# Performance work log

Measured on AMD Instinct MI355X. Metric: run time of the kernel, lower is better.

Reference implementation:

```python
import jax, jax.numpy as jnp
import numpy as np

SEQ, B, H, IN = 512, 64, 1024, 1024
STD = 1.0 / np.sqrt(H)

def setup_inputs() -> dict:
    key = jax.random.key(0)
    ks = jax.random.split(key, 9)
    u = lambda k, shape: jax.random.uniform(k, shape, jnp.float32, -STD, STD)
    return {
        "x": jax.random.normal(ks[0], (SEQ, B, IN), jnp.float32),
        "W_ih0": u(ks[1], (4 * H, IN)),
        "W_hh0": u(ks[2], (4 * H, H)),
        "b_ih0": u(ks[3], (4 * H,)),
        "b_hh0": u(ks[4], (4 * H,)),
        "W_ih1": u(ks[5], (4 * H, H)),
        "W_hh1": u(ks[6], (4 * H, H)),
        "b_ih1": u(ks[7], (4 * H,)),
        "b_hh1": u(ks[8], (4 * H,)),
    }

def _lstm_layer(xs, W_ih, W_hh, b_ih, b_hh):
    # xs: [T, B, in]. Precompute input projections for all steps (one big GEMM),
    # then scan the strictly-sequential recurrence.
    x_proj = jnp.einsum('tbi,gi->tbg', xs, W_ih) + b_ih + b_hh  # [T, B, 4H]
    h0 = jnp.zeros((xs.shape[1], H), xs.dtype)
    c0 = jnp.zeros((xs.shape[1], H), xs.dtype)

    def step(carry, xp):
        h, c = carry
        gates = xp + h @ W_hh.T  # [B, 4H]
        i, f, g, o = jnp.split(gates, 4, axis=1)
        c_next = jax.nn.sigmoid(f) * c + jax.nn.sigmoid(i) * jnp.tanh(g)
        h_next = jax.nn.sigmoid(o) * jnp.tanh(c_next)
        return (h_next, c_next), h_next

    (h_T, c_T), hs = jax.lax.scan(step, (h0, c0), x_proj)
    return hs, h_T, c_T  # hs: [T, B, H]

def reference(x, W_ih0, W_hh0, b_ih0, b_hh0, W_ih1, W_hh1, b_ih1, b_hh1):
    out0, h0, c0 = _lstm_layer(x, W_ih0, W_hh0, b_ih0, b_hh0)
    out1, h1, c1 = _lstm_layer(out0, W_ih1, W_hh1, b_ih1, b_hh1)
    h_n = jnp.stack([h0, h1], axis=0)  # [num_layers, B, H]
    c_n = jnp.stack([c0, c1], axis=0)
    return out1, h_n, c_n
```

## Files before the change

### kernel.cpp

```cpp
#include <hip/hip_runtime.h>

#define T_SEQ 512
#define BATCH 64
#define HDIM 1024
#define G4H 4096
#define TBROWS (T_SEQ * BATCH)
#define NBLK 128
#define UPB 8
#define CNT_STRIDE 16
#define HB (NBLK * BATCH * UPB)

using short8  = __attribute__((ext_vector_type(8))) short;
using float4v = __attribute__((ext_vector_type(4))) float;

__device__ __forceinline__ unsigned short f2bf(float f) {
    union { float f; unsigned int u; } v; v.f = f;
    return (unsigned short)((v.u + 0x7fffu + ((v.u >> 16) & 1u)) >> 16);
}
__device__ __forceinline__ float bf2f(unsigned short b) {
    union { unsigned int u; float f; } v; v.u = ((unsigned int)b) << 16;
    return v.f;
}

__global__ void k_cvt(const float* __restrict__ src, unsigned short* __restrict__ dst, int n) {
    int i = (blockIdx.x * 256 + threadIdx.x) * 4;
    if (i >= n) return;
    float4 v = *(const float4*)(src + i);
    ushort4 o;
    o.x = f2bf(v.x); o.y = f2bf(v.y); o.z = f2bf(v.z); o.w = f2bf(v.w);
    *(ushort4*)(dst + i) = o;
}

__global__ void k_bias(const float* __restrict__ a0, const float* __restrict__ b0,
                       const float* __restrict__ a1, const float* __restrict__ b1,
                       float* __restrict__ s0, float* __restrict__ s1) {
    int t = blockIdx.x * 256 + threadIdx.x;
    if (t < G4H) s0[t] = a0[t] + b0[t];
    else if (t < 2 * G4H) s1[t - G4H] = a1[t - G4H] + b1[t - G4H];
}

__global__ __launch_bounds__(256) void k_gemm_bt(
    const unsigned short* __restrict__ A,
    const unsigned short* __restrict__ B,
    const float* __restrict__ bias,
    unsigned short* __restrict__ C,
    int M, int N, int K)
{
    __shared__ __align__(16) unsigned short Asm[128 * 64];
    __shared__ __align__(16) unsigned short Bsm[128 * 64];

    const int w    = threadIdx.x >> 6;
    const int lane = threadIdx.x & 63;
    const int q    = lane >> 4, r15 = lane & 15;
    const int m0   = blockIdx.y * 128;
    const int n0   = blockIdx.x * 128;
    const int wm   = w & 1, wn = w >> 1;

    float4v acc[4][4];
#pragma unroll
    for (int i = 0; i < 4; i++)
#pragma unroll
        for (int j = 0; j < 4; j++) acc[i][j] = (float4v){0.f, 0.f, 0.f, 0.f};

    for (int k0 = 0; k0 < K; k0 += 64) {
        __syncthreads();
#pragma unroll
        for (int ii = 0; ii < 4; ii++) {
            int plin = (ii * 4 + w) * 64 + lane;
            int row  = plin >> 3;
            int gch  = (plin & 7) ^ (row & 7);
            const unsigned short* ga = A + (size_t)(m0 + row) * K + (k0 + gch * 8);
            const unsigned short* gb = B + (size_t)(n0 + row) * K + (k0 + gch * 8);
            __builtin_amdgcn_global_load_lds((const __attribute__((address_space(1))) void*)ga,
                                             (__attribute__((address_space(3))) void*)(Asm + plin * 8),
                                             16, 0, 0);
            __builtin_amdgcn_global_load_lds((const __attribute__((address_space(1))) void*)gb,
                                             (__attribute__((address_space(3))) void*)(Bsm + plin * 8),
                                             16, 0, 0);
        }
        __syncthreads();
#pragma unroll
        for (int kh = 0; kh < 2; kh++) {
            short8 af[4], bfr[4];
#pragma unroll
            for (int mi = 0; mi < 4; mi++) {
                int row = wm * 64 + mi * 16 + r15;
                int ch  = (kh * 4 + q) ^ (row & 7);
                af[mi]  = *(const short8*)(Asm + (row * 8 + ch) * 8);
            }
#pragma unroll
            for (int ni = 0; ni < 4; ni++) {
                int row = wn * 64 + ni * 16 + r15;
                int ch  = (kh * 4 + q) ^ (row & 7);
                bfr[ni] = *(const short8*)(Bsm + (row * 8 + ch) * 8);
            }
#pragma unroll
            for (int mi = 0; mi < 4; mi++)
#pragma unroll
                for (int ni = 0; ni < 4; ni++)
                    acc[mi][ni] = __builtin_amdgcn_mfma_f32_16x16x32_bf16(af[mi], bfr[ni], acc[mi][ni], 0, 0, 0);
        }
    }

#pragma unroll
    for (int ni = 0; ni < 4; ni++) {
        int col  = n0 + wn * 64 + ni * 16 + r15;
        float bv = bias[col];
#pragma unroll
        for (int mi = 0; mi < 4; mi++) {
            int rowb = m0 + wm * 64 + mi * 16 + q * 4;
#pragma unroll
            for (int rr = 0; rr < 4; rr++)
                C[(size_t)(rowb + rr) * N + col] = f2bf(acc[mi][ni][rr] + bv);
        }
    }
}

#define LD16U(dst, ptr) \
    asm volatile("global_load_dwordx4 %0, %1, off sc0 sc1" : "=v"(dst) : "v"(ptr))
#define ST16U(ptr, val) \
    asm volatile("global_store_dwordx4 %0, %1, off sc0 sc1" :: "v"(ptr), "v"(val) : "memory")

#define VMWAIT(N) do { \
    asm volatile("s_waitcnt vmcnt(" #N ")" ::: "memory"); \
    __builtin_amdgcn_sched_barrier(0); \
} while (0)

__device__ __forceinline__ void gate(const unsigned* prod, int g, unsigned tgt, int lane) {
    if (lane < 32) {
        const unsigned* f = prod + (size_t)(g * 32 + lane) * CNT_STRIDE;
        while (__hip_atomic_load(f, __ATOMIC_RELAXED, __HIP_MEMORY_SCOPE_AGENT) < tgt)
            __builtin_amdgcn_s_sleep(1);
    }
    __builtin_amdgcn_sched_barrier(0);
}

__device__ __forceinline__ void issue_grp(const unsigned short* hb, const unsigned short* lb,
                                          short8 (&H)[8], short8 (&L)[8]) {
#pragma unroll
    for (int i = 0; i < 8; i++) {
        LD16U(H[i], hb + i * 2048);
        LD16U(L[i], lb + i * 2048);
    }
}

__device__ __forceinline__ void mfma_grp(int g, const short8 (&ah)[8], const short8 (&al)[8],
                                         const unsigned short* Whi, const unsigned short* Wlo,
                                         int q, int r15, float4v (&acc)[2][3])
{
#pragma unroll
    for (int i = 0; i < 8; i++) {
        const int kc = g * 8 + i;
#pragma unroll
        for (int jg = 0; jg < 2; jg++) {
            const unsigned short* bb = Whi + jg * 16 * HDIM + (kc * 4 + q) * 128 + r15 * 8;
            const unsigned short* bl = Wlo + jg * 16 * HDIM + (kc * 4 + q) * 128 + r15 * 8;
            short8 bh  = *(const short8*)bb;
            short8 blv = *(const short8*)bl;
            acc[jg][0] = __builtin_amdgcn_mfma_f32_16x16x32_bf16(ah[i], bh,  acc[jg][0], 0, 0, 0);
            acc[jg][1] = __builtin_amdgcn_mfma_f32_16x16x32_bf16(al[i], bh,  acc[jg][1], 0, 0, 0);
            acc[jg][2] = __builtin_amdgcn_mfma_f32_16x16x32_bf16(ah[i], blv, acc[jg][2], 0, 0, 0);
        }
    }
}

__global__ __launch_bounds__(256) void k_lstm(
    const float* __restrict__ Whh,
    const unsigned short* __restrict__ xproj,
    unsigned short* __restrict__ h_hi,
    unsigned short* __restrict__ h_lo,
    unsigned short* __restrict__ out_b,
    float* __restrict__ out_f,
    float* __restrict__ hn, float* __restrict__ cn,
    unsigned* __restrict__ bar,
    int bar_base)
{
    extern __shared__ char smem[];
    unsigned short* Whi = (unsigned short*)smem;
    unsigned short* Wlo = Whi + 32 * HDIM;
    float* glds         = (float*)(Wlo + 32 * HDIM);
    unsigned short* stg_hi = (unsigned short*)(glds + 64 * 33);
    unsigned short* stg_lo = stg_hi + 64 * 8;

    const int nb   = blockIdx.x;
    const int tid  = threadIdx.x;
    const int w    = tid >> 6;
    const int lane = tid & 63;
    const int q    = lane >> 4, r15 = lane & 15;
    const int brow = w * 16 + r15;

    unsigned* prod = bar;
    unsigned* done = bar + NBLK * CNT_STRIDE;

    {
        int j    = tid >> 3;
        int g    = j >> 3, ui = j & 7;
        int jg   = j >> 4, jloc = j & 15;
        size_t grow = (size_t)(g * HDIM + nb * UPB + ui) * HDIM;
        unsigned short* whiB = Whi + jg * 16 * HDIM;
        unsigned short* wloB = Wlo + jg * 16 * HDIM;
        int kbase = (tid & 7) * 128;
        for (int e = 0; e < 128; e += 4) {
            int k = kbase + e;
            float4 wv = *(const float4*)(Whh + grow + k);
            float vv[4] = {wv.x, wv.y, wv.z, wv.w};
            unsigned short hs[4], ls[4];
#pragma unroll
            for (int m = 0; m < 4; m++) {
                hs[m] = f2bf(vv[m]);
                ls[m] = f2bf(vv[m] - bf2f(hs[m]));
            }
            int addr = (k >> 3) * 128 + jloc * 8 + (k & 7);
            *(ushort4*)(whiB + addr) = (ushort4){hs[0], hs[1], hs[2], hs[3]};
            *(ushort4*)(wloB + addr) = (ushort4){ls[0], ls[1], ls[2], ls[3]};
        }
    }

    const int b_act = tid >> 2;
    const int u0    = (tid & 3) * 2;
    float c0 = 0.f, c1 = 0.f;

    ushort2 xpv[4];
    {
        const unsigned short* xpb = xproj + (size_t)b_act * G4H + nb * UPB + u0;
#pragma unroll
        for (int g = 0; g < 4; g++) xpv[g] = *(const ushort2*)(xpb + g * HDIM);
    }

    __syncthreads();

    for (int t = 0; t < T_SEQ; t++) {
        const int cur = t & 1, nxt = cur ^ 1;
        const unsigned tgt = (unsigned)(bar_base + t);

        unsigned done_pre = NBLK;
        if (t >= 2 && tid < 64)
            done_pre = __hip_atomic_load(done + (size_t)(bar_base + t - 1) * CNT_STRIDE,
                                         __ATOMIC_RELAXED, __HIP_MEMORY_SCOPE_AGENT);

        float4v acc[2][3];
#pragma unroll
        for (int jg = 0; jg < 2; jg++)
#pragma unroll
            for (int p = 0; p < 3; p++) acc[jg][p] = (float4v){0.f, 0.f, 0.f, 0.f};

        if (t > 0) {
            const unsigned short* hbase = h_hi + (size_t)cur * HB + q * 512 + brow * 8;
            const unsigned short* lbase = h_lo + (size_t)cur * HB + q * 512 + brow * 8;
            short8 H0[8], L0[8], H1[8], L1[8];
            const int g0 = nb & 3;
            const int gA = g0, gB = (g0 + 1) & 3, gC = (g0 + 2) & 3, gD = (g0 + 3) & 3;

            gate(prod, gA, tgt, lane);
            issue_grp(hbase + gA * 16384, lbase + gA * 16384, H0, L0);
            gate(prod, gB, tgt, lane);
            issue_grp(hbase + gB * 16384, lbase + gB * 16384, H1, L1);
            VMWAIT(16);
            mfma_grp(gA, H0, L0, Whi, Wlo, q, r15, acc);
            gate(prod, gC, tgt, lane);
            issue_grp(hbase + gC * 16384, lbase + gC * 16384, H0, L0);
            VMWAIT(16);
            mfma_grp(gB, H1, L1, Whi, Wlo, q, r15, acc);
            gate(prod, gD, tgt, lane);
            issue_grp(hbase + gD * 16384, lbase + gD * 16384, H1, L1);
            VMWAIT(16);
            mfma_grp(gC, H0, L0, Whi, Wlo, q, r15, acc);
            VMWAIT(0);
            mfma_grp(gD, H1, L1, Whi, Wlo, q, r15, acc);
        }

#pragma unroll
        for (int jg = 0; jg < 2; jg++) {
            int browg = w * 16 + q * 4;
#pragma unroll
            for (int rr = 0; rr < 4; rr++)
                glds[(browg + rr) * 33 + jg * 16 + r15] = acc[jg][0][rr] + acc[jg][1][rr] + acc[jg][2][rr];
        }
        __syncthreads();

        if (t > 0 && tid == 0)
            __hip_atomic_fetch_add(done + (size_t)(bar_base + t) * CNT_STRIDE, 1u,
                                   __ATOMIC_RELAXED, __HIP_MEMORY_SCOPE_AGENT);

        float hv0, hv1;
        {
            const float* gr = glds + b_act * 33;
            float gi0 = gr[0*8 + u0]     + bf2f(xpv[0].x);
            float gi1 = gr[0*8 + u0 + 1] + bf2f(xpv[0].y);
            float gf0 = gr[1*8 + u0]     + bf2f(xpv[1].x);
            float gf1 = gr[1*8 + u0 + 1] + bf2f(xpv[1].y);
            float gg0 = gr[2*8 + u0]     + bf2f(xpv[2].x);
            float gg1 = gr[2*8 + u0 + 1] + bf2f(xpv[2].y);
            float go0 = gr[3*8 + u0]     + bf2f(xpv[3].x);
            float go1 = gr[3*8 + u0 + 1] + bf2f(xpv[3].y);

            c0 = (1.f / (1.f + __expf(-gf0))) * c0 + (1.f / (1.f + __expf(-gi0))) * tanhf(gg0);
            c1 = (1.f / (1.f + __expf(-gf1))) * c1 + (1.f / (1.f + __expf(-gi1))) * tanhf(gg1);
            hv0 = (1.f / (1.f + __expf(-go0))) * tanhf(c0);
            hv1 = (1.f / (1.f + __expf(-go1))) * tanhf(c1);
        }
        unsigned short hb0 = f2bf(hv0), hb1 = f2bf(hv1);

        if (t == T_SEQ - 1) {
            size_t ooff = ((size_t)t * BATCH + b_act) * HDIM + nb * UPB + u0;
            if (out_b) *(ushort2*)(out_b + ooff) = (ushort2){hb0, hb1};
            if (out_f) *(float2*)(out_f + ooff) = (float2){hv0, hv1};
            int hidx = b_act * HDIM + nb * UPB + u0;
            hn[hidx] = hv0; hn[hidx + 1] = hv1;
            cn[hidx] = c0;  cn[hidx + 1] = c1;
            break;
        }

        *(ushort2*)(stg_hi + b_act * 8 + u0) = (ushort2){hb0, hb1};
        *(ushort2*)(stg_lo + b_act * 8 + u0) =
            (ushort2){f2bf(hv0 - bf2f(hb0)), f2bf(hv1 - bf2f(hb1))};
        __syncthreads();

        if (tid < 64) {
            while (done_pre < (unsigned)NBLK) {
                __builtin_amdgcn_s_sleep(1);
                done_pre = __hip_atomic_load(done + (size_t)(bar_base + t - 1) * CNT_STRIDE,
                                             __ATOMIC_RELAXED, __HIP_MEMORY_SCOPE_AGENT);
            }
            __builtin_amdgcn_sched_barrier(0);
            short8 sh = *(const short8*)(stg_hi + tid * 8);
            short8 sl = *(const short8*)(stg_lo + tid * 8);
            unsigned short* dh = h_hi + (size_t)nxt * HB + nb * 512 + tid * 8;
            unsigned short* dl = h_lo + (size_t)nxt * HB + nb * 512 + tid * 8;
            ST16U(dh, sh);
            ST16U(dl, sl);
            asm volatile("s_waitcnt vmcnt(0)" ::: "memory");
            __builtin_amdgcn_sched_barrier(0);
            if (tid == 0)
                __hip_atomic_store(prod + (size_t)nb * CNT_STRIDE, tgt + 1,
                                   __ATOMIC_RELAXED, __HIP_MEMORY_SCOPE_AGENT);
        }

        {
            size_t ooff = ((size_t)t * BATCH + b_act) * HDIM + nb * UPB + u0;
            if (out_b) *(ushort2*)(out_b + ooff) = (ushort2){hb0, hb1};
            if (out_f) *(float2*)(out_f + ooff) = (float2){hv0, hv1};
        }

        {
            const unsigned short* xpb = xproj + ((size_t)(t + 1) * BATCH + b_act) * G4H + nb * UPB + u0;
#pragma unroll
            for (int g = 0; g < 4; g++) xpv[g] = *(const ushort2*)(xpb + g * HDIM);
        }
    }
}

extern "C" void kernel_launch(void* const* d_in, const int* in_sizes, int n_in,
                              void* d_out, int out_size, void* d_ws, size_t ws_size,
                              hipStream_t stream) {
    (void)in_sizes; (void)n_in; (void)out_size; (void)ws_size;
    const float* x    = (const float*)d_in[0];
    const float* Wih0 = (const float*)d_in[1];
    const float* Whh0 = (const float*)d_in[2];
    const float* bih0 = (const float*)d_in[3];
    const float* bhh0 = (const float*)d_in[4];
    const float* Wih1 = (const float*)d_in[5];
    const float* Whh1 = (const float*)d_in[6];
    const float* bih1 = (const float*)d_in[7];
    const float* bhh1 = (const float*)d_in[8];
    float* out = (float*)d_out;

    unsigned short* xb0   = (unsigned short*)d_ws;
    unsigned short* xb1   = xb0 + (size_t)TBROWS * HDIM;
    unsigned short* wb0   = xb1 + (size_t)TBROWS * HDIM;
    unsigned short* wb1   = wb0 + (size_t)G4H * HDIM;
    unsigned short* xproj = wb1 + (size_t)G4H * HDIM;
    unsigned short* hhi   = xproj + (size_t)TBROWS * G4H;
    unsigned short* hlo   = hhi + 2 * HB;
    float* bsum0          = (float*)(hlo + 2 * HB);
    float* bsum1          = bsum0 + G4H;
    unsigned* bar         = (unsigned*)(bsum1 + G4H);

    float* hn0 = out + (size_t)TBROWS * HDIM;
    float* hn1 = hn0 + BATCH * HDIM;
    float* cn0 = hn1 + BATCH * HDIM;
    float* cn1 = cn0 + BATCH * HDIM;

    const unsigned lstm_lds = 32 * HDIM * 2 * 2 + 64 * 33 * 4 + 2 * 64 * 8 * 2;
    static bool attr_set = false;
    if (!attr_set) {
        hipFuncSetAttribute((const void*)k_lstm,
                            hipFuncAttributeMaxDynamicSharedMemorySize, lstm_lds);
        attr_set = true;
    }

    hipMemsetAsync(bar, 0, (NBLK + 2 * T_SEQ) * CNT_STRIDE * sizeof(unsigned), stream);

    k_cvt<<<(TBROWS * HDIM / 4 + 255) / 256, 256, 0, stream>>>(x, xb0, TBROWS * HDIM);
    k_cvt<<<(G4H * HDIM / 4 + 255) / 256, 256, 0, stream>>>(Wih0, wb0, G4H * HDIM);
    k_cvt<<<(G4H * HDIM / 4 + 255) / 256, 256, 0, stream>>>(Wih1, wb1, G4H * HDIM);
    k_bias<<<(2 * G4H + 255) / 256, 256, 0, stream>>>(bih0, bhh0, bih1, bhh1, bsum0, bsum1);

    dim3 gg(G4H / 128, TBROWS / 128);

    k_gemm_bt<<<gg, 256, 0, stream>>>(xb0, wb0, bsum0, xproj, TBROWS, G4H, HDIM);
    {
        const float* whh = Whh0;
        const unsigned short* xp = xproj;
        unsigned short* hh = hhi; unsigned short* hl = hlo;
        unsigned short* ob = xb1;
        float* of = nullptr;
        float* hn = hn0; float* cn = cn0;
        unsigned* bp = bar; int bb = 0;
        void* args[] = {(void*)&whh, (void*)&xp, (void*)&hh, (void*)&hl,
                        (void*)&ob, (void*)&of, (void*)&hn, (void*)&cn,
                        (void*)&bp, (void*)&bb};
        hipLaunchCooperativeKernel((void*)k_lstm, dim3(NBLK), dim3(256), args, lstm_lds, stream);
    }

    k_gemm_bt<<<gg, 256, 0, stream>>>(xb1, wb1, bsum1, xproj, TBROWS, G4H, HDIM);
    {
        const float* whh = Whh1;
        const unsigned short* xp = xproj;
        unsigned short* hh = hhi; unsigned short* hl = hlo;
        unsigned short* ob = nullptr;
        float* of = out;
        float* hn = hn1; float* cn = cn1;
        unsigned* bp = bar; int bb = T_SEQ;
        void* args[] = {(void*)&whh, (void*)&xp, (void*)&hh, (void*)&hl,
                        (void*)&ob, (void*)&of, (void*)&hn, (void*)&cn,
                        (void*)&bp, (void*)&bb};
        hipLaunchCooperativeKernel((void*)k_lstm, dim3(NBLK), dim3(256), args, lstm_lds, stream);
    }
}
```

Before: 8.763 ms.

## Write h directly from all threads and pack producer flags densely

Drops the LDS staging buffer and the single-wavefront store. Every thread now writes its packed bf16 hi/lo pair straight to global memory, waits on vmcnt, and then a block barrier runs before thread 0 publishes the producer flag. The producer flags lose their per-flag stride and become contiguous, so a consumer's 32 lanes poll adjacent words instead of spread cache lines. All threads also poll the done counter rather than one wavefront. The aim is to shorten the per-step publish critical path, at the cost of narrower stores and more polling traffic.

```diff
diff --git a/kernel.cpp b/kernel.cpp
--- a/kernel.cpp
+++ b/kernel.cpp
@@ -118,8 +118,8 @@
 
 #define LD16U(dst, ptr) \
     asm volatile("global_load_dwordx4 %0, %1, off sc0 sc1" : "=v"(dst) : "v"(ptr))
-#define ST16U(ptr, val) \
-    asm volatile("global_store_dwordx4 %0, %1, off sc0 sc1" :: "v"(ptr), "v"(val) : "memory")
+#define ST4U(ptr, val) \
+    asm volatile("global_store_dword %0, %1, off sc0 sc1" :: "v"(ptr), "v"(val) : "memory")
 
 #define VMWAIT(N) do { \
     asm volatile("s_waitcnt vmcnt(" #N ")" ::: "memory"); \
@@ -128,7 +128,7 @@
 
 __device__ __forceinline__ void gate(const unsigned* prod, int g, unsigned tgt, int lane) {
     if (lane < 32) {
-        const unsigned* f = prod + (size_t)(g * 32 + lane) * CNT_STRIDE;
+        const unsigned* f = prod + g * 32 + lane;
         while (__hip_atomic_load(f, __ATOMIC_RELAXED, __HIP_MEMORY_SCOPE_AGENT) < tgt)
             __builtin_amdgcn_s_sleep(1);
     }
@@ -179,8 +179,6 @@
     unsigned short* Whi = (unsigned short*)smem;
     unsigned short* Wlo = Whi + 32 * HDIM;
     float* glds         = (float*)(Wlo + 32 * HDIM);
-    unsigned short* stg_hi = (unsigned short*)(glds + 64 * 33);
-    unsigned short* stg_lo = stg_hi + 64 * 8;
 
     const int nb   = blockIdx.x;
     const int tid  = threadIdx.x;
@@ -190,7 +188,7 @@
     const int brow = w * 16 + r15;
 
     unsigned* prod = bar;
-    unsigned* done = bar + NBLK * CNT_STRIDE;
+    unsigned* done = bar + NBLK;
 
     {
         int j    = tid >> 3;
@@ -234,7 +232,7 @@
         const unsigned tgt = (unsigned)(bar_base + t);
 
         unsigned done_pre = NBLK;
-        if (t >= 2 && tid < 64)
+        if (t >= 2)
             done_pre = __hip_atomic_load(done + (size_t)(bar_base + t - 1) * CNT_STRIDE,
                                          __ATOMIC_RELAXED, __HIP_MEMORY_SCOPE_AGENT);
 
@@ -311,30 +309,29 @@
             break;
         }
 
-        *(ushort2*)(stg_hi + b_act * 8 + u0) = (ushort2){hb0, hb1};
-        *(ushort2*)(stg_lo + b_act * 8 + u0) =
-            (ushort2){f2bf(hv0 - bf2f(hb0)), f2bf(hv1 - bf2f(hb1))};
-        __syncthreads();
-
-        if (tid < 64) {
+        if (t >= 2) {
             while (done_pre < (unsigned)NBLK) {
                 __builtin_amdgcn_s_sleep(1);
                 done_pre = __hip_atomic_load(done + (size_t)(bar_base + t - 1) * CNT_STRIDE,
                                              __ATOMIC_RELAXED, __HIP_MEMORY_SCOPE_AGENT);
             }
-            __builtin_amdgcn_sched_barrier(0);
-            short8 sh = *(const short8*)(stg_hi + tid * 8);
-            short8 sl = *(const short8*)(stg_lo + tid * 8);
-            unsigned short* dh = h_hi + (size_t)nxt * HB + nb * 512 + tid * 8;
-            unsigned short* dl = h_lo + (size_t)nxt * HB + nb * 512 + tid * 8;
-            ST16U(dh, sh);
-            ST16U(dl, sl);
-            asm volatile("s_waitcnt vmcnt(0)" ::: "memory");
-            __builtin_amdgcn_sched_barrier(0);
-            if (tid == 0)
-                __hip_atomic_store(prod + (size_t)nb * CNT_STRIDE, tgt + 1,
-                                   __ATOMIC_RELAXED, __HIP_MEMORY_SCOPE_AGENT);
-        }
+        }
+        __builtin_amdgcn_sched_barrier(0);
+
+        {
+            unsigned short lb0 = f2bf(hv0 - bf2f(hb0)), lb1 = f2bf(hv1 - bf2f(hb1));
+            unsigned hpack = (unsigned)hb0 | ((unsigned)hb1 << 16);
+            unsigned lpack = (unsigned)lb0 | ((unsigned)lb1 << 16);
+            unsigned short* dh = h_hi + (size_t)nxt * HB + nb * 512 + tid * 2;
+            unsigned short* dl = h_lo + (size_t)nxt * HB + nb * 512 + tid * 2;
+            ST4U(dh, hpack);
+            ST4U(dl, lpack);
+        }
+        asm volatile("s_waitcnt vmcnt(0)" ::: "memory");
+        __builtin_amdgcn_sched_barrier(0);
+        __syncthreads();
+        if (tid == 0)
+            __hip_atomic_store(prod + nb, tgt + 1, __ATOMIC_RELAXED, __HIP_MEMORY_SCOPE_AGENT);
 
         {
             size_t ooff = ((size_t)t * BATCH + b_act) * HDIM + nb * UPB + u0;
@@ -381,7 +378,7 @@
     float* cn0 = hn1 + BATCH * HDIM;
     float* cn1 = cn0 + BATCH * HDIM;
 
-    const unsigned lstm_lds = 32 * HDIM * 2 * 2 + 64 * 33 * 4 + 2 * 64 * 8 * 2;
+    const unsigned lstm_lds = 32 * HDIM * 2 * 2 + 64 * 33 * 4;
     static bool attr_set = false;
     if (!attr_set) {
         hipFuncSetAttribute((const void*)k_lstm,
@@ -389,7 +386,7 @@
         attr_set = true;
     }
 
-    hipMemsetAsync(bar, 0, (NBLK + 2 * T_SEQ) * CNT_STRIDE * sizeof(unsigned), stream);
+    hipMemsetAsync(bar, 0, (NBLK + 2 * T_SEQ * CNT_STRIDE) * sizeof(unsigned), stream);
 
     k_cvt<<<(TBROWS * HDIM / 4 + 255) / 256, 256, 0, stream>>>(x, xb0, TBROWS * HDIM);
     k_cvt<<<(G4H * HDIM / 4 + 255) / 256, 256, 0, stream>>>(Wih0, wb0, G4H * HDIM);
```

After: 8.581 ms. 2.1% less time.
